# Kernel tuning notes

Hardware: AMD Instinct MI355X
Metric: run time of the kernel (lower is better)

Reference implementation:

```python
import jax, jax.numpy as jnp
import numpy as np

TAU = 2.0          # LIF membrane time constant (init kwarg)
ALPHA = 2.0        # spikingjelly surrogate.ATan default alpha
V_TH = 1.0         # spikingjelly LIFNode default v_threshold

# Heaviside spike with ATan surrogate gradient (spikingjelly semantics)
@jax.custom_vjp
def spike(v):
    return (v >= V_TH).astype(v.dtype)

def _spike_fwd(v):
    return spike(v), v

def _spike_bwd(v, g):
    sg = (ALPHA / 2.0) / (1.0 + (jnp.pi / 2.0 * ALPHA * (v - V_TH)) ** 2)
    return (g * sg,)

spike.defvjp(_spike_fwd, _spike_bwd)

def lif(x):
    # Fresh LIFNode: v_prev = 0, v_reset = 0, decay_input=True
    # charge: v = v_prev + (x - (v_prev - v_reset)) / tau  ->  v = x / tau
    return spike(x / TAU)

def setup_inputs() -> dict:
    key = jax.random.key(0)
    ks = jax.random.split(key, 5)
    B = 2097152
    # kaiming-uniform-ish scale: 1/sqrt(fan_in)
    def w(k, out_f, in_f):
        return jax.random.normal(k, (out_f, in_f), dtype=jnp.float32) / np.sqrt(in_f)
    return {
        "x": jax.random.normal(ks[0], (B, 5), dtype=jnp.float32),
        "W1": w(ks[1], 32, 5),
        "W2": w(ks[2], 32, 32),
        "W3": w(ks[3], 16, 32),
        "W4": w(ks[4], 10, 16),
    }

def reference(x, W1, W2, W3, W4):
    # fc: Linear(5,32)->LIF -> Linear(32,32)->LIF -> Linear(32,16)->LIF
    s = lif(x @ W1.T)          # [B, 32]
    s = lif(s @ W2.T)          # [B, 32]
    s = lif(s @ W3.T)          # [B, 16]
    # fc1: Linear(16,10)->LIF
    return lif(s @ W4.T)       # [B, 10]
```

## Files before the change

### kernel.cpp

```cpp
#include <hip/hip_runtime.h>


typedef float v4f __attribute__((ext_vector_type(4)));
typedef float v2f __attribute__((ext_vector_type(2)));

#define TPB 256
#define RPL 2
#define WROWS (64 * RPL)
#define RPB (TPB * RPL)

__global__ __launch_bounds__(64) void snn_prep(
    const float* __restrict__ W1,
    const float* __restrict__ W2,
    float* __restrict__ ws)
{
    const int t = threadIdx.x;
    float mm = -3.4e38f;
    if (t < 32) {
#pragma unroll
        for (int k = 0; k < 5; ++k) ws[k * 32 + t] = W1[t * 5 + k];
        mm = W2[t];
#pragma unroll
        for (int j = 1; j < 32; ++j) mm = fmaxf(mm, W2[j * 32 + t]);
        ws[160 + t] = mm;
    }
#pragma unroll
    for (int off = 32; off; off >>= 1) mm = fmaxf(mm, __shfl_xor(mm, off));
    if (t == 0) ws[192] = mm;
}

__global__ __launch_bounds__(TPB) void snn_fused(
    const float* __restrict__ x,
    const float* __restrict__ W2,
    const float* __restrict__ W3,
    const float* __restrict__ W4,
    const float* __restrict__ ws,
    float* __restrict__ out,
    int B)
{
    __shared__ __align__(16) float stage[4][WROWS * 10];

    const int t = threadIdx.x;
    const int wv = t >> 6, lane = t & 63;
    float* sbuf = stage[wv];
    const long wrow0 = (long)blockIdx.x * RPB + (long)wv * WROWS;
    if (wrow0 >= B) return;

    const v2f* __restrict__ w1p = (const v2f*)ws;
    const float* __restrict__ smx = ws + 160;
    const float mxmax = ws[192];

    if (wrow0 + WROWS <= B) {
        const v4f* xg = (const v4f*)(x + wrow0 * 5);
        v4f* s4 = (v4f*)sbuf;
#pragma unroll
        for (int e = 0; e < 3; ++e) {
            int idx = e * 64 + lane;
            if (idx < (WROWS * 5) / 4) s4[idx] = xg[idx];
        }

        v2f xp[5];
        {
            const v2f* sx = (const v2f*)(sbuf + lane * 10);
#pragma unroll
            for (int e = 0; e < 5; ++e) xp[e] = sx[e];
        }
        const float* xf = (const float*)xp;

        unsigned m[RPL] = {0u, 0u};
#pragma unroll
        for (int j2 = 0; j2 < 16; ++j2) {
            const v2f wa = w1p[j2], wb = w1p[16 + j2], wc = w1p[32 + j2];
            const v2f wd = w1p[48 + j2], we = w1p[64 + j2];
#pragma unroll
            for (int c = 0; c < RPL; ++c) {
                v2f h = xf[c * 5 + 0] * wa;
                h += xf[c * 5 + 1] * wb;
                h += xf[c * 5 + 2] * wc;
                h += xf[c * 5 + 3] * wd;
                h += xf[c * 5 + 4] * we;
                if (h.x >= 2.0f) m[c] |= (1u << (2 * j2));
                if (h.y >= 2.0f) m[c] |= (1u << (2 * j2 + 1));
            }
        }

        bool dense[RPL];
        unsigned m2s[RPL];
        bool any_dense = false;
#pragma unroll
        for (int c = 0; c < RPL; ++c) {
            dense[c] = false;
            m2s[c] = 0u;
            const unsigned mc = m[c];
            if (mc && ((float)__popc(mc) * mxmax >= 1.998f)) {
                float S = 0.0f;
                unsigned mm = mc;
                while (mm) { int i = __ffs(mm) - 1; mm &= mm - 1; S += smx[i]; }
                if (S >= 1.998f) {
                    float h2[32];
#pragma unroll
                    for (int j = 0; j < 32; ++j) h2[j] = 0.0f;
                    mm = mc;
                    while (mm) {
                        const int i = __ffs(mm) - 1;
                        mm &= mm - 1;
                        const float* col = W2 + i;
#pragma unroll
                        for (int j = 0; j < 32; ++j) h2[j] += col[j * 32];
                    }
                    unsigned m2 = 0u;
#pragma unroll
                    for (int j = 0; j < 32; ++j)
                        if (h2[j] >= 2.0f) m2 |= (1u << j);
                    m2s[c] = m2;
                    if (m2) { dense[c] = true; any_dense = true; }
                }
            }
        }

        if (!__any(any_dense)) {
            v4f z = {0.0f, 0.0f, 0.0f, 0.0f};
            v4f* og = (v4f*)(out + wrow0 * 10);
#pragma unroll
            for (int e = 0; e < 5; ++e)
                og[e * 64 + lane] = z;
        } else {
            {
                v4f z = {0.0f, 0.0f, 0.0f, 0.0f};
#pragma unroll
                for (int e = 0; e < 5; ++e) s4[e * 64 + lane] = z;
            }
#pragma unroll
            for (int c = 0; c < RPL; ++c) {
                if (!dense[c]) continue;
                const unsigned m2 = m2s[c];
                unsigned m3 = 0u;
#pragma unroll
                for (int j = 0; j < 16; ++j) {
                    float g = 0.0f;
#pragma unroll
                    for (int i = 0; i < 32; ++i)
                        if ((m2 >> i) & 1u) g += W3[j * 32 + i];
                    if (g >= 2.0f) m3 |= (1u << j);
                }
                float* orow = sbuf + (lane * RPL + c) * 10;
#pragma unroll
                for (int j = 0; j < 10; ++j) {
                    float g = 0.0f;
#pragma unroll
                    for (int i = 0; i < 16; ++i)
                        if ((m3 >> i) & 1u) g += W4[j * 16 + i];
                    orow[j] = (g >= 2.0f) ? 1.0f : 0.0f;
                }
            }
            v4f* og = (v4f*)(out + wrow0 * 10);
            const v4f* s4c = (const v4f*)sbuf;
#pragma unroll
            for (int e = 0; e < 5; ++e)
                og[e * 64 + lane] = s4c[e * 64 + lane];
        }
    } else {
        for (int c = 0; c < RPL; ++c) {
            const long r = wrow0 + (long)lane * RPL + c;
            if (r >= B) continue;
            float xr[5];
#pragma unroll
            for (int k = 0; k < 5; ++k) xr[k] = x[r * 5 + k];
            unsigned mc = 0u;
#pragma unroll
            for (int j2 = 0; j2 < 16; ++j2) {
                v2f h = xr[0] * w1p[j2];
                h += xr[1] * w1p[16 + j2];
                h += xr[2] * w1p[32 + j2];
                h += xr[3] * w1p[48 + j2];
                h += xr[4] * w1p[64 + j2];
                if (h.x >= 2.0f) mc |= (1u << (2 * j2));
                if (h.y >= 2.0f) mc |= (1u << (2 * j2 + 1));
            }
            float o[10];
#pragma unroll
            for (int j = 0; j < 10; ++j) o[j] = 0.0f;
            if (mc && ((float)__popc(mc) * mxmax >= 1.998f)) {
                float S = 0.0f;
                unsigned mm = mc;
                while (mm) { int i = __ffs(mm) - 1; mm &= mm - 1; S += smx[i]; }
                if (S >= 1.998f) {
                    float h2[32];
#pragma unroll
                    for (int j = 0; j < 32; ++j) h2[j] = 0.0f;
                    mm = mc;
                    while (mm) {
                        const int i = __ffs(mm) - 1;
                        mm &= mm - 1;
                        const float* col = W2 + i;
#pragma unroll
                        for (int j = 0; j < 32; ++j) h2[j] += col[j * 32];
                    }
                    unsigned m2 = 0u;
#pragma unroll
                    for (int j = 0; j < 32; ++j)
                        if (h2[j] >= 2.0f) m2 |= (1u << j);
                    if (m2) {
                        unsigned m3 = 0u;
#pragma unroll
                        for (int j = 0; j < 16; ++j) {
                            float g = 0.0f;
#pragma unroll
                            for (int i = 0; i < 32; ++i)
                                if ((m2 >> i) & 1u) g += W3[j * 32 + i];
                            if (g >= 2.0f) m3 |= (1u << j);
                        }
#pragma unroll
                        for (int j = 0; j < 10; ++j) {
                            float g = 0.0f;
#pragma unroll
                            for (int i = 0; i < 16; ++i)
                                if ((m3 >> i) & 1u) g += W4[j * 16 + i];
                            o[j] = (g >= 2.0f) ? 1.0f : 0.0f;
                        }
                    }
                }
            }
#pragma unroll
            for (int j = 0; j < 10; ++j) out[r * 10 + j] = o[j];
        }
    }
}

extern "C" void kernel_launch(void* const* d_in, const int* in_sizes, int n_in,
                              void* d_out, int out_size, void* d_ws, size_t ws_size,
                              hipStream_t stream) {
    const float* x  = (const float*)d_in[0];
    const float* W1 = (const float*)d_in[1];
    const float* W2 = (const float*)d_in[2];
    const float* W3 = (const float*)d_in[3];
    const float* W4 = (const float*)d_in[4];
    float* out = (float*)d_out;
    float* ws  = (float*)d_ws;

    int B = in_sizes[0] / 5;
    snn_prep<<<1, 64, 0, stream>>>(W1, W2, ws);
    int grid = (B + RPB - 1) / RPB;
    snn_fused<<<grid, TPB, 0, stream>>>(x, W2, W3, W4, ws, out, B);
}
```

Measured before the change: 165.9 us.

## Fuse prep into main kernel and software-pipeline x loads across tiles

Removes the separate prep kernel launch and computes the W2 column maxima per wave in shared memory inside the main kernel. W1 is now read directly from global instead of from a transposed workspace. Each block processes four tiles, prefetching the next tile's x into registers while the current one is computed, to hide load latency. Dense rows now write outputs directly with scalar stores instead of staging through LDS. The cost is redundant per-block W2 max computation, fewer blocks, and uncoalesced output stores on the dense path.

```diff
diff --git a/kernel.cpp b/kernel.cpp
--- a/kernel.cpp
+++ b/kernel.cpp
@@ -6,176 +6,188 @@
 
 #define TPB 256
 #define RPL 2
-#define WROWS (64 * RPL)
-#define RPB (TPB * RPL)
-
-__global__ __launch_bounds__(64) void snn_prep(
+#define TROWS (64 * RPL)
+#define TILE (TPB * RPL)
+#define NTILES 4
+#define BROWS (TILE * NTILES)
+
+__global__ __launch_bounds__(TPB) void snn_all(
+    const float* __restrict__ x,
     const float* __restrict__ W1,
-    const float* __restrict__ W2,
-    float* __restrict__ ws)
-{
-    const int t = threadIdx.x;
-    float mm = -3.4e38f;
-    if (t < 32) {
-#pragma unroll
-        for (int k = 0; k < 5; ++k) ws[k * 32 + t] = W1[t * 5 + k];
-        mm = W2[t];
-#pragma unroll
-        for (int j = 1; j < 32; ++j) mm = fmaxf(mm, W2[j * 32 + t]);
-        ws[160 + t] = mm;
-    }
-#pragma unroll
-    for (int off = 32; off; off >>= 1) mm = fmaxf(mm, __shfl_xor(mm, off));
-    if (t == 0) ws[192] = mm;
-}
-
-__global__ __launch_bounds__(TPB) void snn_fused(
-    const float* __restrict__ x,
     const float* __restrict__ W2,
     const float* __restrict__ W3,
     const float* __restrict__ W4,
-    const float* __restrict__ ws,
     float* __restrict__ out,
     int B)
 {
-    __shared__ __align__(16) float stage[4][WROWS * 10];
+    __shared__ __align__(16) float xs[4][2][TROWS * 5];
+    __shared__ float smxl[4][32];
 
     const int t = threadIdx.x;
     const int wv = t >> 6, lane = t & 63;
-    float* sbuf = stage[wv];
-    const long wrow0 = (long)blockIdx.x * RPB + (long)wv * WROWS;
-    if (wrow0 >= B) return;
-
-    const v2f* __restrict__ w1p = (const v2f*)ws;
-    const float* __restrict__ smx = ws + 160;
-    const float mxmax = ws[192];
-
-    if (wrow0 + WROWS <= B) {
-        const v4f* xg = (const v4f*)(x + wrow0 * 5);
-        v4f* s4 = (v4f*)sbuf;
+    const long blk0 = (long)blockIdx.x * BROWS;
+    if (blk0 >= B) return;
+
+    const bool fullblk = (blk0 + BROWS <= B);
+
+    v4f g[3];
+    if (fullblk) {
+        const v4f* xg = (const v4f*)(x + (blk0 + (long)wv * TROWS) * 5);
 #pragma unroll
         for (int e = 0; e < 3; ++e) {
             int idx = e * 64 + lane;
-            if (idx < (WROWS * 5) / 4) s4[idx] = xg[idx];
+            if (idx < (TROWS * 5) / 4) g[e] = xg[idx];
         }
-
-        v2f xp[5];
-        {
-            const v2f* sx = (const v2f*)(sbuf + lane * 10);
-#pragma unroll
-            for (int e = 0; e < 5; ++e) xp[e] = sx[e];
-        }
-        const float* xf = (const float*)xp;
-
-        unsigned m[RPL] = {0u, 0u};
-#pragma unroll
-        for (int j2 = 0; j2 < 16; ++j2) {
-            const v2f wa = w1p[j2], wb = w1p[16 + j2], wc = w1p[32 + j2];
-            const v2f wd = w1p[48 + j2], we = w1p[64 + j2];
+    }
+
+    const int col = lane & 31;
+    float cm = W2[col];
+#pragma unroll
+    for (int j = 1; j < 32; ++j) cm = fmaxf(cm, W2[j * 32 + col]);
+    smxl[wv][col] = cm;
+    float mxmax = cm;
+#pragma unroll
+    for (int off = 16; off; off >>= 1)
+        mxmax = fmaxf(mxmax, __shfl_xor(mxmax, off, 32));
+    const float* __restrict__ smx = smxl[wv];
+
+    if (fullblk) {
+        for (int tt = 0; tt < NTILES; ++tt) {
+            const long wt0 = blk0 + (long)tt * TILE + (long)wv * TROWS;
+            float* sb = xs[wv][tt & 1];
+            v4f* s4 = (v4f*)sb;
+
+#pragma unroll
+            for (int e = 0; e < 3; ++e) {
+                int idx = e * 64 + lane;
+                if (idx < (TROWS * 5) / 4) s4[idx] = g[e];
+            }
+
+            if (tt + 1 < NTILES) {
+                const v4f* xg =
+                    (const v4f*)(x + (blk0 + (long)(tt + 1) * TILE +
+                                      (long)wv * TROWS) * 5);
+#pragma unroll
+                for (int e = 0; e < 3; ++e) {
+                    int idx = e * 64 + lane;
+                    if (idx < (TROWS * 5) / 4) g[e] = xg[idx];
+                }
+            }
+
+            v2f xp[5];
+            {
+                const v2f* sx = (const v2f*)(sb + lane * 10);
+#pragma unroll
+                for (int e = 0; e < 5; ++e) xp[e] = sx[e];
+            }
+            const float* xf = (const float*)xp;
+
+            unsigned m[RPL] = {0u, 0u};
+#pragma unroll
+            for (int j = 0; j < 32; ++j) {
+                const float* w = W1 + j * 5;
+#pragma unroll
+                for (int c = 0; c < RPL; ++c) {
+                    float h = xf[c * 5 + 0] * w[0];
+                    h += xf[c * 5 + 1] * w[1];
+                    h += xf[c * 5 + 2] * w[2];
+                    h += xf[c * 5 + 3] * w[3];
+                    h += xf[c * 5 + 4] * w[4];
+                    if (h >= 2.0f) m[c] |= (1u << j);
+                }
+            }
+
+            bool dense[RPL];
+            unsigned m2s[RPL];
+            bool any_dense = false;
 #pragma unroll
             for (int c = 0; c < RPL; ++c) {
-                v2f h = xf[c * 5 + 0] * wa;
-                h += xf[c * 5 + 1] * wb;
-                h += xf[c * 5 + 2] * wc;
-                h += xf[c * 5 + 3] * wd;
-                h += xf[c * 5 + 4] * we;
-                if (h.x >= 2.0f) m[c] |= (1u << (2 * j2));
-                if (h.y >= 2.0f) m[c] |= (1u << (2 * j2 + 1));
-            }
-        }
-
-        bool dense[RPL];
-        unsigned m2s[RPL];
-        bool any_dense = false;
-#pragma unroll
-        for (int c = 0; c < RPL; ++c) {
-            dense[c] = false;
-            m2s[c] = 0u;
-            const unsigned mc = m[c];
-            if (mc && ((float)__popc(mc) * mxmax >= 1.998f)) {
-                float S = 0.0f;
-                unsigned mm = mc;
-                while (mm) { int i = __ffs(mm) - 1; mm &= mm - 1; S += smx[i]; }
-                if (S >= 1.998f) {
-                    float h2[32];
-#pragma unroll
-                    for (int j = 0; j < 32; ++j) h2[j] = 0.0f;
-                    mm = mc;
-                    while (mm) {
-                        const int i = __ffs(mm) - 1;
-                        mm &= mm - 1;
-                        const float* col = W2 + i;
-#pragma unroll
-                        for (int j = 0; j < 32; ++j) h2[j] += col[j * 32];
-                    }
-                    unsigned m2 = 0u;
-#pragma unroll
-                    for (int j = 0; j < 32; ++j)
-                        if (h2[j] >= 2.0f) m2 |= (1u << j);
-                    m2s[c] = m2;
-                    if (m2) { dense[c] = true; any_dense = true; }
-                }
-            }
-        }
-
-        if (!__any(any_dense)) {
-            v4f z = {0.0f, 0.0f, 0.0f, 0.0f};
-            v4f* og = (v4f*)(out + wrow0 * 10);
-#pragma unroll
-            for (int e = 0; e < 5; ++e)
-                og[e * 64 + lane] = z;
-        } else {
-            {
+                dense[c] = false;
+                m2s[c] = 0u;
+                const unsigned mc = m[c];
+                if (mc && ((float)__popc(mc) * mxmax >= 1.998f)) {
+                    float S = 0.0f;
+                    unsigned mm = mc;
+                    while (mm) { int i = __ffs(mm) - 1; mm &= mm - 1; S += smx[i]; }
+                    if (S >= 1.998f) {
+                        float h2[32];
+#pragma unroll
+                        for (int j = 0; j < 32; ++j) h2[j] = 0.0f;
+                        mm = mc;
+                        while (mm) {
+                            const int i = __ffs(mm) - 1;
+                            mm &= mm - 1;
+                            const float* colp = W2 + i;
+#pragma unroll
+                            for (int j = 0; j < 32; ++j) h2[j] += colp[j * 32];
+                        }
+                        unsigned m2 = 0u;
+#pragma unroll
+                        for (int j = 0; j < 32; ++j)
+                            if (h2[j] >= 2.0f) m2 |= (1u << j);
+                        m2s[c] = m2;
+                        if (m2) { dense[c] = true; any_dense = true; }
+                    }
+                }
+            }
+
+            if (!__any(any_dense)) {
                 v4f z = {0.0f, 0.0f, 0.0f, 0.0f};
-#pragma unroll
-                for (int e = 0; e < 5; ++e) s4[e * 64 + lane] = z;
-            }
-#pragma unroll
-            for (int c = 0; c < RPL; ++c) {
-                if (!dense[c]) continue;
-                const unsigned m2 = m2s[c];
-                unsigned m3 = 0u;
-#pragma unroll
-                for (int j = 0; j < 16; ++j) {
-                    float g = 0.0f;
-#pragma unroll
-                    for (int i = 0; i < 32; ++i)
-                        if ((m2 >> i) & 1u) g += W3[j * 32 + i];
-                    if (g >= 2.0f) m3 |= (1u << j);
-                }
-                float* orow = sbuf + (lane * RPL + c) * 10;
-#pragma unroll
-                for (int j = 0; j < 10; ++j) {
-                    float g = 0.0f;
-#pragma unroll
-                    for (int i = 0; i < 16; ++i)
-                        if ((m3 >> i) & 1u) g += W4[j * 16 + i];
-                    orow[j] = (g >= 2.0f) ? 1.0f : 0.0f;
-                }
-            }
-            v4f* og = (v4f*)(out + wrow0 * 10);
-            const v4f* s4c = (const v4f*)sbuf;
-#pragma unroll
-            for (int e = 0; e < 5; ++e)
-                og[e * 64 + lane] = s4c[e * 64 + lane];
+                v4f* og = (v4f*)(out + wt0 * 10);
+#pragma unroll
+                for (int e = 0; e < 5; ++e) og[e * 64 + lane] = z;
+            } else {
+                float oo[RPL][10];
+#pragma unroll
+                for (int c = 0; c < RPL; ++c)
+#pragma unroll
+                    for (int j = 0; j < 10; ++j) oo[c][j] = 0.0f;
+#pragma unroll
+                for (int c = 0; c < RPL; ++c) {
+                    if (!dense[c]) continue;
+                    const unsigned m2 = m2s[c];
+                    unsigned m3 = 0u;
+#pragma unroll
+                    for (int j = 0; j < 16; ++j) {
+                        float gg = 0.0f;
+#pragma unroll
+                        for (int i = 0; i < 32; ++i)
+                            if ((m2 >> i) & 1u) gg += W3[j * 32 + i];
+                        if (gg >= 2.0f) m3 |= (1u << j);
+                    }
+#pragma unroll
+                    for (int j = 0; j < 10; ++j) {
+                        float gg = 0.0f;
+#pragma unroll
+                        for (int i = 0; i < 16; ++i)
+                            if ((m3 >> i) & 1u) gg += W4[j * 16 + i];
+                        oo[c][j] = (gg >= 2.0f) ? 1.0f : 0.0f;
+                    }
+                }
+#pragma unroll
+                for (int c = 0; c < RPL; ++c) {
+                    float* orow = out + (wt0 + (long)lane * RPL + c) * 10;
+#pragma unroll
+                    for (int j = 0; j < 10; ++j) orow[j] = oo[c][j];
+                }
+            }
         }
     } else {
-        for (int c = 0; c < RPL; ++c) {
-            const long r = wrow0 + (long)lane * RPL + c;
-            if (r >= B) continue;
+        const long rend = (blk0 + BROWS < (long)B) ? blk0 + BROWS : (long)B;
+        for (long r = blk0 + t; r < rend; r += TPB) {
             float xr[5];
 #pragma unroll
             for (int k = 0; k < 5; ++k) xr[k] = x[r * 5 + k];
             unsigned mc = 0u;
 #pragma unroll
-            for (int j2 = 0; j2 < 16; ++j2) {
-                v2f h = xr[0] * w1p[j2];
-                h += xr[1] * w1p[16 + j2];
-                h += xr[2] * w1p[32 + j2];
-                h += xr[3] * w1p[48 + j2];
-                h += xr[4] * w1p[64 + j2];
-                if (h.x >= 2.0f) mc |= (1u << (2 * j2));
-                if (h.y >= 2.0f) mc |= (1u << (2 * j2 + 1));
+            for (int j = 0; j < 32; ++j) {
+                const float* w = W1 + j * 5;
+                float h = xr[0] * w[0];
+                h += xr[1] * w[1];
+                h += xr[2] * w[2];
+                h += xr[3] * w[3];
+                h += xr[4] * w[4];
+                if (h >= 2.0f) mc |= (1u << j);
             }
             float o[10];
 #pragma unroll
@@ -192,9 +204,9 @@
                     while (mm) {
                         const int i = __ffs(mm) - 1;
                         mm &= mm - 1;
-                        const float* col = W2 + i;
-#pragma unroll
-                        for (int j = 0; j < 32; ++j) h2[j] += col[j * 32];
+                        const float* colp = W2 + i;
+#pragma unroll
+                        for (int j = 0; j < 32; ++j) h2[j] += colp[j * 32];
                     }
                     unsigned m2 = 0u;
 #pragma unroll
@@ -204,19 +216,19 @@
                         unsigned m3 = 0u;
 #pragma unroll
                         for (int j = 0; j < 16; ++j) {
-                            float g = 0.0f;
+                            float gg = 0.0f;
 #pragma unroll
                             for (int i = 0; i < 32; ++i)
-                                if ((m2 >> i) & 1u) g += W3[j * 32 + i];
-                            if (g >= 2.0f) m3 |= (1u << j);
+                                if ((m2 >> i) & 1u) gg += W3[j * 32 + i];
+                            if (gg >= 2.0f) m3 |= (1u << j);
                         }
 #pragma unroll
                         for (int j = 0; j < 10; ++j) {
-                            float g = 0.0f;
+                            float gg = 0.0f;
 #pragma unroll
                             for (int i = 0; i < 16; ++i)
-                                if ((m3 >> i) & 1u) g += W4[j * 16 + i];
-                            o[j] = (g >= 2.0f) ? 1.0f : 0.0f;
+                                if ((m3 >> i) & 1u) gg += W4[j * 16 + i];
+                            o[j] = (gg >= 2.0f) ? 1.0f : 0.0f;
                         }
                     }
                 }
@@ -236,10 +248,8 @@
     const float* W3 = (const float*)d_in[3];
     const float* W4 = (const float*)d_in[4];
     float* out = (float*)d_out;
-    float* ws  = (float*)d_ws;
 
     int B = in_sizes[0] / 5;
-    snn_prep<<<1, 64, 0, stream>>>(W1, W2, ws);
-    int grid = (B + RPB - 1) / RPB;
-    snn_fused<<<grid, TPB, 0, stream>>>(x, W2, W3, W4, ws, out, B);
+    int grid = (B + BROWS - 1) / BROWS;
+    snn_all<<<grid, TPB, 0, stream>>>(x, W1, W2, W3, W4, out, B);
 }
```

New measurement: 175.9 us. 1.06x slower.
